# Kernel optimization log

Measured on AMD Instinct MI355X. Metric: run time of the kernel, lower is better.

The kernel has to match this reference:

```python
import jax, jax.numpy as jnp
import numpy as np

NFIELD, NKER = 8, 16
B, Y, X, P, T = 32, 32, 32, 16, 8


def setup_inputs() -> dict:
    key = jax.random.key(0)
    k1, k2 = jax.random.split(key)
    fieldpatch = jax.random.normal(k1, (B, NFIELD, Y, X, P, T), dtype=jnp.float32)
    quadpatch = jax.random.uniform(k2, (B, Y, X, P, T), dtype=jnp.float32)
    zeros_fk = jnp.zeros((NFIELD, NKER), dtype=jnp.float32)
    return {
        "fieldpatch": fieldpatch,
        "quadpatch": quadpatch,
        "mean_lat": zeros_fk, "logstd_lat": zeros_fk,
        "mean_lon": zeros_fk, "logstd_lon": zeros_fk,
        "mean_lev": zeros_fk, "logstd_lev": zeros_fk,
        "logtau_time": zeros_fk,
    }


def _gaussian1d(mean, logstd, length):
    # (f, k, length): exp(-0.5*((coord - mean)/std)^2), coord in [-1, 1]
    coord = jnp.linspace(-1.0, 1.0, length, dtype=mean.dtype)
    std = jnp.exp(logstd)
    z = (coord[None, None, :] - mean[..., None]) / std[..., None]
    return jnp.exp(-0.5 * z * z)


def _exponential1d(logtau, length):
    # (f, k, length): exp(-coord / tau), coord = 0..length-1
    coord = jnp.arange(length, dtype=logtau.dtype)
    tau = jnp.exp(logtau) + 1e-4
    return jnp.exp(-coord[None, None, :] / tau[..., None])


def reference(fieldpatch, quadpatch, mean_lat, logstd_lat, mean_lon, logstd_lon,
              mean_lev, logstd_lev, logtau_time):
    b, f, y, x, p, t = fieldpatch.shape
    ky = _gaussian1d(mean_lat, logstd_lat, y)      # (f,k,y)
    kx = _gaussian1d(mean_lon, logstd_lon, x)      # (f,k,x)
    kp = _gaussian1d(mean_lev, logstd_lev, p)      # (f,k,p)
    kt = _exponential1d(logtau_time, t)            # (f,k,t)
    # Separable outer product -> full kernel (f,k,y,x,p,t)
    kernel = jnp.einsum('fky,fkx,fkp,fkt->fkyxpt', ky, kx, kp, kt)
    qmean = quadpatch.mean(axis=0)                 # (y,x,p,t)
    integral = jnp.einsum('fkyxpt,yxpt->fk', kernel, qmean) + 1e-4
    weights = kernel / integral[:, :, None, None, None, None]
    # torch weights() runs under @torch.no_grad(): weights are constant wrt autograd
    weights = jax.lax.stop_gradient(weights)
    features = jnp.einsum('bfyxpt,fkyxpt,byxpt->bfk', fieldpatch, weights, quadpatch)
    return features.reshape(b, -1)
```

## Files before the change

### kernel.cpp

```cpp
#include <hip/hip_runtime.h>
#include <math.h>

#define NF 8
#define NK 16
#define BB 32
#define YY 32
#define XX 32
#define PP 16
#define TT 8
#define YX (YY*XX)
#define PT (PP*TT)
#define YXPT (YX*PT)
#define CHUNKS 8
#define COLS_PER_BLOCK (YX/CHUNKS)
#define COLS_PER_WAVE  (COLS_PER_BLOCK/4)
#define MAIN_ITERS     (COLS_PER_WAVE/2)

#define WPT_OFF   0
#define WYX_OFF   (NF*NK*PT)
#define QMEAN_OFF (WYX_OFF + NF*YX*NK)
#define ACC_OFF   (QMEAN_OFF + YXPT)
#define INTG_OFF  (ACC_OFF + CHUNKS*BB*NF*NK)

__global__ __launch_bounds__(256) void k_prep(const float* __restrict__ quad,
                       const float* __restrict__ mean_lat, const float* __restrict__ logstd_lat,
                       const float* __restrict__ mean_lon, const float* __restrict__ logstd_lon,
                       const float* __restrict__ mean_lev, const float* __restrict__ logstd_lev,
                       const float* __restrict__ logtau,
                       float* __restrict__ ws) {
    const int tid = threadIdx.x, bx = blockIdx.x;

    if (bx < 512) {
        __shared__ float4 sm[256];
        const int j4 = bx * 64 + (tid & 63);
        const int bg = tid >> 6;
        const float4* q4 = (const float4*)quad;
        float4 a = make_float4(0.f, 0.f, 0.f, 0.f);
        #pragma unroll
        for (int i = 0; i < 8; ++i) {
            float4 v = q4[(size_t)(bg * 8 + i) * (YXPT / 4) + j4];
            a.x += v.x; a.y += v.y; a.z += v.z; a.w += v.w;
        }
        sm[tid] = a;
        __syncthreads();
        if (tid < 64) {
            float4 r0 = sm[tid], r1 = sm[tid + 64], r2 = sm[tid + 128], r3 = sm[tid + 192];
            float4 r;
            r.x = (r0.x + r1.x + r2.x + r3.x) * (1.f / BB);
            r.y = (r0.y + r1.y + r2.y + r3.y) * (1.f / BB);
            r.z = (r0.z + r1.z + r2.z + r3.z) * (1.f / BB);
            r.w = (r0.w + r1.w + r2.w + r3.w) * (1.f / BB);
            ((float4*)(ws + QMEAN_OFF))[j4] = r;
        }
        return;
    }
    const int fk = bx - 512;
    if (tid >= 128) return;
    const int f = fk >> 4, k = fk & 15;
    const float mlat = mean_lat[fk], slat = expf(logstd_lat[fk]);
    const float mlon = mean_lon[fk], slon = expf(logstd_lon[fk]);
    const float mlev = mean_lev[fk], slev = expf(logstd_lev[fk]);
    const float tau  = expf(logtau[fk]) + 1e-4f;

    {
        const int p = tid >> 3, t = tid & 7;
        const float cp = -1.f + 2.f * (float)p / (PP - 1);
        const float zp = (cp - mlev) / slev;
        ws[WPT_OFF + fk * PT + tid] = expf(-0.5f * zp * zp) * expf(-(float)t / tau);
    }
    #pragma unroll
    for (int i = 0; i < 8; ++i) {
        const int yx = i * 128 + tid;
        const int y = yx >> 5, x = yx & 31;
        const float cy = -1.f + 2.f * (float)y / (YY - 1);
        const float cx = -1.f + 2.f * (float)x / (XX - 1);
        const float zy = (cy - mlat) / slat;
        const float zx = (cx - mlon) / slon;
        ws[WYX_OFF + (f * YX + yx) * NK + k] = expf(-0.5f * zy * zy) * expf(-0.5f * zx * zx);
    }
}

__global__ __launch_bounds__(256) void k_integral(float* __restrict__ ws) {
    const int fk = blockIdx.x >> 2, qr = blockIdx.x & 3;
    const int tid = threadIdx.x;
    const int f = fk >> 4, k = fk & 15;
    const int yx = qr * 256 + tid;
    const float4* w4 = (const float4*)(ws + WPT_OFF + fk * PT);
    const float4* q4 = (const float4*)(ws + QMEAN_OFF + (size_t)yx * PT);
    float s = 0.f;
    #pragma unroll
    for (int j = 0; j < PT / 4; ++j) {
        float4 w = w4[j], q = q4[j];
        s += w.x * q.x + w.y * q.y + w.z * q.z + w.w * q.w;
    }
    float partial = ws[WYX_OFF + (f * YX + yx) * NK + k] * s;
    #pragma unroll
    for (int m = 32; m; m >>= 1) partial += __shfl_xor(partial, m);
    __shared__ float red[4];
    if ((tid & 63) == 0) red[tid >> 6] = partial;
    __syncthreads();
    if (tid == 0)
        ws[INTG_OFF + qr * (NF * NK) + fk] = red[0] + red[1] + red[2] + red[3];
}

__global__ __launch_bounds__(256, 3) void k_main(const float* __restrict__ field,
                                                 const float* __restrict__ quad,
                                                 float* __restrict__ ws) {
    const int bx = blockIdx.x;
    const int f = bx & 7, chunk = (bx >> 3) & 7, b = bx >> 6;
    const int tid = threadIdx.x;
    const int wave = tid >> 6, L = tid & 63;
    const int half = L >> 5, qg = L & 31;

    __shared__ float sw[COLS_PER_BLOCK * NK];
    {
        const float4* src = (const float4*)(ws + WYX_OFF + (size_t)(f * YX + chunk * COLS_PER_BLOCK) * NK);
        float4* dst = (float4*)sw;
        dst[tid] = src[tid];
        dst[tid + 256] = src[tid + 256];
    }

    float4 wf[NK];
    #pragma unroll
    for (int k = 0; k < NK; ++k)
        wf[k] = *(const float4*)(ws + WPT_OFF + (f * NK + k) * PT + 4 * qg);

    float acc[NK];
    #pragma unroll
    for (int k = 0; k < NK; ++k) acc[k] = 0.f;

    const int colBase = chunk * COLS_PER_BLOCK + wave * COLS_PER_WAVE;
    const float4* fp = (const float4*)(field + (size_t)(b * NF + f) * YXPT + (size_t)colBase * PT + 4 * L);
    const float4* qp = (const float4*)(quad + (size_t)b * YXPT + (size_t)colBase * PT + 4 * L);
    const int STEP = (2 * PT) / 4;

    __syncthreads();
    const float* swc = sw + (wave * COLS_PER_WAVE + half) * NK;

    float4 fa = fp[0];
    float4 qa = qp[0];
    float4 fb = fp[STEP];
    float4 qb = qp[STEP];
    float4 fc = fp[2 * STEP];
    float4 qc = qp[2 * STEP];

    #pragma unroll 1
    for (int s = 0; s < MAIN_ITERS; ++s) {
        const int sn = (s + 3 < MAIN_ITERS) ? (s + 3) : 0;
        float4 fd = fp[sn * STEP];
        float4 qd = qp[sn * STEP];

        float4 ga;
        ga.x = fa.x * qa.x; ga.y = fa.y * qa.y; ga.z = fa.z * qa.z; ga.w = fa.w * qa.w;

        const float4* wvp = (const float4*)(swc + s * 2 * NK);
        #pragma unroll
        for (int j = 0; j < 4; ++j) {
            float4 w = wvp[j];
            {
                const int k = 4 * j;
                float d = ga.x * wf[k].x;
                d = fmaf(ga.y, wf[k].y, d);
                d = fmaf(ga.z, wf[k].z, d);
                d = fmaf(ga.w, wf[k].w, d);
                acc[k] = fmaf(w.x, d, acc[k]);
            }
            {
                const int k = 4 * j + 1;
                float d = ga.x * wf[k].x;
                d = fmaf(ga.y, wf[k].y, d);
                d = fmaf(ga.z, wf[k].z, d);
                d = fmaf(ga.w, wf[k].w, d);
                acc[k] = fmaf(w.y, d, acc[k]);
            }
            {
                const int k = 4 * j + 2;
                float d = ga.x * wf[k].x;
                d = fmaf(ga.y, wf[k].y, d);
                d = fmaf(ga.z, wf[k].z, d);
                d = fmaf(ga.w, wf[k].w, d);
                acc[k] = fmaf(w.z, d, acc[k]);
            }
            {
                const int k = 4 * j + 3;
                float d = ga.x * wf[k].x;
                d = fmaf(ga.y, wf[k].y, d);
                d = fmaf(ga.z, wf[k].z, d);
                d = fmaf(ga.w, wf[k].w, d);
                acc[k] = fmaf(w.w, d, acc[k]);
            }
        }
        fa = fb; qa = qb;
        fb = fc; qb = qc;
        fc = fd; qc = qd;
    }

    __shared__ float red[4][NK];
    #pragma unroll
    for (int k = 0; k < NK; ++k) {
        float v = acc[k];
        v += __shfl_xor(v, 32); v += __shfl_xor(v, 16); v += __shfl_xor(v, 8);
        v += __shfl_xor(v, 4);  v += __shfl_xor(v, 2);  v += __shfl_xor(v, 1);
        if (L == 0) red[wave][k] = v;
    }
    __syncthreads();
    if (tid < NK) {
        float s2 = red[0][tid] + red[1][tid] + red[2][tid] + red[3][tid];
        ws[ACC_OFF + chunk * (BB * NF * NK) + (b * NF + f) * NK + tid] = s2;
    }
}

__global__ void k_final(const float* __restrict__ ws, float* __restrict__ out) {
    int i = blockIdx.x * 256 + threadIdx.x;
    if (i >= BB * NF * NK) return;
    float a = 0.f;
    #pragma unroll
    for (int c = 0; c < CHUNKS; ++c) a += ws[ACC_OFF + c * (BB * NF * NK) + i];
    const int fk = i & (NF * NK - 1);
    float g = 1e-4f;
    #pragma unroll
    for (int q = 0; q < 4; ++q) g += ws[INTG_OFF + q * (NF * NK) + fk];
    out[i] = a / g;
}

extern "C" void kernel_launch(void* const* d_in, const int* in_sizes, int n_in,
                              void* d_out, int out_size, void* d_ws, size_t ws_size,
                              hipStream_t stream) {
    const float* field = (const float*)d_in[0];
    const float* quad  = (const float*)d_in[1];
    float* ws = (float*)d_ws;

    k_prep<<<640, 256, 0, stream>>>(quad,
        (const float*)d_in[2], (const float*)d_in[3],
        (const float*)d_in[4], (const float*)d_in[5],
        (const float*)d_in[6], (const float*)d_in[7],
        (const float*)d_in[8], ws);
    k_integral<<<NF * NK * 4, 256, 0, stream>>>(ws);
    k_main<<<BB * NF * CHUNKS, 256, 0, stream>>>(field, quad, ws);
    k_final<<<(BB * NF * NK + 255) / 256, 256, 0, stream>>>(ws, (float*)d_out);
}
```

Before: 238.6 us.

## Fuse kernel generation and normalization integral into main reduction kernel

```diff
diff --git a/kernel.cpp b/kernel.cpp
--- a/kernel.cpp
+++ b/kernel.cpp
@@ -15,212 +15,157 @@
 #define COLS_PER_BLOCK (YX/CHUNKS)
 #define COLS_PER_WAVE  (COLS_PER_BLOCK/4)
 #define MAIN_ITERS     (COLS_PER_WAVE/2)
+#define STEP           ((2*PT)/4)
 
-#define WPT_OFF   0
-#define WYX_OFF   (NF*NK*PT)
-#define QMEAN_OFF (WYX_OFF + NF*YX*NK)
-#define ACC_OFF   (QMEAN_OFF + YXPT)
-#define INTG_OFF  (ACC_OFF + CHUNKS*BB*NF*NK)
+#define ACC_OFF   0
+#define ACCQ_OFF  (CHUNKS*BB*NF*NK)
 
-__global__ __launch_bounds__(256) void k_prep(const float* __restrict__ quad,
-                       const float* __restrict__ mean_lat, const float* __restrict__ logstd_lat,
-                       const float* __restrict__ mean_lon, const float* __restrict__ logstd_lon,
-                       const float* __restrict__ mean_lev, const float* __restrict__ logstd_lev,
-                       const float* __restrict__ logtau,
-                       float* __restrict__ ws) {
-    const int tid = threadIdx.x, bx = blockIdx.x;
 
-    if (bx < 512) {
-        __shared__ float4 sm[256];
-        const int j4 = bx * 64 + (tid & 63);
-        const int bg = tid >> 6;
-        const float4* q4 = (const float4*)quad;
-        float4 a = make_float4(0.f, 0.f, 0.f, 0.f);
-        #pragma unroll
-        for (int i = 0; i < 8; ++i) {
-            float4 v = q4[(size_t)(bg * 8 + i) * (YXPT / 4) + j4];
-            a.x += v.x; a.y += v.y; a.z += v.z; a.w += v.w;
-        }
-        sm[tid] = a;
-        __syncthreads();
-        if (tid < 64) {
-            float4 r0 = sm[tid], r1 = sm[tid + 64], r2 = sm[tid + 128], r3 = sm[tid + 192];
-            float4 r;
-            r.x = (r0.x + r1.x + r2.x + r3.x) * (1.f / BB);
-            r.y = (r0.y + r1.y + r2.y + r3.y) * (1.f / BB);
-            r.z = (r0.z + r1.z + r2.z + r3.z) * (1.f / BB);
-            r.w = (r0.w + r1.w + r2.w + r3.w) * (1.f / BB);
-            ((float4*)(ws + QMEAN_OFF))[j4] = r;
-        }
-        return;
-    }
-    const int fk = bx - 512;
-    if (tid >= 128) return;
-    const int f = fk >> 4, k = fk & 15;
-    const float mlat = mean_lat[fk], slat = expf(logstd_lat[fk]);
-    const float mlon = mean_lon[fk], slon = expf(logstd_lon[fk]);
-    const float mlev = mean_lev[fk], slev = expf(logstd_lev[fk]);
-    const float tau  = expf(logtau[fk]) + 1e-4f;
+#define KQ(WC, K) do {                                                          \
+    float d  = ga.x * wf[K].x; d  = fmaf(ga.y, wf[K].y, d );                    \
+    d  = fmaf(ga.z, wf[K].z, d ); d  = fmaf(ga.w, wf[K].w, d );                 \
+    float dq = qa.x * wf[K].x; dq = fmaf(qa.y, wf[K].y, dq);                    \
+    dq = fmaf(qa.z, wf[K].z, dq); dq = fmaf(qa.w, wf[K].w, dq);                 \
+    acc[K]  = fmaf(WC, d,  acc[K]);                                             \
+    accq[K] = fmaf(WC, dq, accq[K]);                                            \
+} while (0)
 
-    {
-        const int p = tid >> 3, t = tid & 7;
-        const float cp = -1.f + 2.f * (float)p / (PP - 1);
-        const float zp = (cp - mlev) / slev;
-        ws[WPT_OFF + fk * PT + tid] = expf(-0.5f * zp * zp) * expf(-(float)t / tau);
-    }
-    #pragma unroll
-    for (int i = 0; i < 8; ++i) {
-        const int yx = i * 128 + tid;
-        const int y = yx >> 5, x = yx & 31;
-        const float cy = -1.f + 2.f * (float)y / (YY - 1);
-        const float cx = -1.f + 2.f * (float)x / (XX - 1);
-        const float zy = (cy - mlat) / slat;
-        const float zx = (cx - mlon) / slon;
-        ws[WYX_OFF + (f * YX + yx) * NK + k] = expf(-0.5f * zy * zy) * expf(-0.5f * zx * zx);
-    }
-}
+#define COLPAIR_COMPUTE(WVP) do {                                               \
+    float4 ga;                                                                  \
+    ga.x = fa.x*qa.x; ga.y = fa.y*qa.y; ga.z = fa.z*qa.z; ga.w = fa.w*qa.w;     \
+    float4 w0 = (WVP)[0], w1 = (WVP)[1], w2 = (WVP)[2], w3 = (WVP)[3];          \
+    KQ(w0.x, 0);  KQ(w0.y, 1);  KQ(w0.z, 2);  KQ(w0.w, 3);                      \
+    KQ(w1.x, 4);  KQ(w1.y, 5);  KQ(w1.z, 6);  KQ(w1.w, 7);                      \
+    KQ(w2.x, 8);  KQ(w2.y, 9);  KQ(w2.z, 10); KQ(w2.w, 11);                     \
+    KQ(w3.x, 12); KQ(w3.y, 13); KQ(w3.z, 14); KQ(w3.w, 15);                     \
+} while (0)
 
-__global__ __launch_bounds__(256) void k_integral(float* __restrict__ ws) {
-    const int fk = blockIdx.x >> 2, qr = blockIdx.x & 3;
-    const int tid = threadIdx.x;
-    const int f = fk >> 4, k = fk & 15;
-    const int yx = qr * 256 + tid;
-    const float4* w4 = (const float4*)(ws + WPT_OFF + fk * PT);
-    const float4* q4 = (const float4*)(ws + QMEAN_OFF + (size_t)yx * PT);
-    float s = 0.f;
-    #pragma unroll
-    for (int j = 0; j < PT / 4; ++j) {
-        float4 w = w4[j], q = q4[j];
-        s += w.x * q.x + w.y * q.y + w.z * q.z + w.w * q.w;
-    }
-    float partial = ws[WYX_OFF + (f * YX + yx) * NK + k] * s;
-    #pragma unroll
-    for (int m = 32; m; m >>= 1) partial += __shfl_xor(partial, m);
-    __shared__ float red[4];
-    if ((tid & 63) == 0) red[tid >> 6] = partial;
-    __syncthreads();
-    if (tid == 0)
-        ws[INTG_OFF + qr * (NF * NK) + fk] = red[0] + red[1] + red[2] + red[3];
-}
-
-__global__ __launch_bounds__(256, 3) void k_main(const float* __restrict__ field,
-                                                 const float* __restrict__ quad,
-                                                 float* __restrict__ ws) {
+__global__ __launch_bounds__(256, 3) void k_main(
+    const float* __restrict__ field, const float* __restrict__ quad,
+    const float* __restrict__ mean_lat, const float* __restrict__ logstd_lat,
+    const float* __restrict__ mean_lon, const float* __restrict__ logstd_lon,
+    const float* __restrict__ mean_lev, const float* __restrict__ logstd_lev,
+    const float* __restrict__ logtau, float* __restrict__ ws)
+{
     const int bx = blockIdx.x;
     const int f = bx & 7, chunk = (bx >> 3) & 7, b = bx >> 6;
     const int tid = threadIdx.x;
     const int wave = tid >> 6, L = tid & 63;
     const int half = L >> 5, qg = L & 31;
 
-    __shared__ float sw[COLS_PER_BLOCK * NK];
-    {
-        const float4* src = (const float4*)(ws + WYX_OFF + (size_t)(f * YX + chunk * COLS_PER_BLOCK) * NK);
-        float4* dst = (float4*)sw;
-        dst[tid] = src[tid];
-        dst[tid + 256] = src[tid + 256];
+    const int colBase = chunk * COLS_PER_BLOCK + wave * COLS_PER_WAVE;
+    const float4* fp = (const float4*)(field + (size_t)(b * NF + f) * YXPT + (size_t)colBase * PT) + L;
+    const float4* qp = (const float4*)(quad  + (size_t)b * YXPT            + (size_t)colBase * PT) + L;
+
+    float4 fbuf[4], qbuf[4];
+    #pragma unroll
+    for (int j = 0; j < 4; ++j) { fbuf[j] = fp[j * STEP]; qbuf[j] = qp[j * STEP]; }
+
+    __shared__ __align__(16) float sw[COLS_PER_BLOCK * NK];
+    __shared__ __align__(16) float spt[NK * PT];
+    __shared__ float prm[NK][8];
+
+    if (tid < NK) {
+        const int fk = f * NK + tid;
+        prm[tid][0] = mean_lat[fk];
+        prm[tid][1] = expf(-logstd_lat[fk]);
+        prm[tid][2] = mean_lon[fk];
+        prm[tid][3] = expf(-logstd_lon[fk]);
+        prm[tid][4] = mean_lev[fk];
+        prm[tid][5] = expf(-logstd_lev[fk]);
+        prm[tid][6] = 1.f / (expf(logtau[fk]) + 1e-4f);
     }
+    __syncthreads();
+
+    #pragma unroll
+    for (int i = 0; i < 8; ++i) {
+        const int e = i * 256 + tid;
+        const int col = e >> 4, k = e & 15;
+        const int yx = chunk * COLS_PER_BLOCK + col;
+        const float cy = -1.f + 2.f * (float)(yx >> 5) / (YY - 1);
+        const float cx = -1.f + 2.f * (float)(yx & 31) / (XX - 1);
+        const float zy = (cy - prm[k][0]) * prm[k][1];
+        const float zx = (cx - prm[k][2]) * prm[k][3];
+        sw[col * NK + k] = expf(-0.5f * (zy * zy + zx * zx));
+    }
+    #pragma unroll
+    for (int i = 0; i < 8; ++i) {
+        const int e = i * 256 + tid;
+        const int k = e >> 7, pt = e & 127;
+        const float cp = -1.f + 2.f * (float)(pt >> 3) / (PP - 1);
+        const float zp = (cp - prm[k][4]) * prm[k][5];
+        spt[e] = expf(-0.5f * zp * zp - (float)(pt & 7) * prm[k][6]);
+    }
+    __syncthreads();
 
     float4 wf[NK];
     #pragma unroll
-    for (int k = 0; k < NK; ++k)
-        wf[k] = *(const float4*)(ws + WPT_OFF + (f * NK + k) * PT + 4 * qg);
+    for (int k = 0; k < NK; ++k) wf[k] = ((const float4*)(spt + k * PT))[qg];
 
-    float acc[NK];
+    float acc[NK], accq[NK];
     #pragma unroll
-    for (int k = 0; k < NK; ++k) acc[k] = 0.f;
+    for (int k = 0; k < NK; ++k) { acc[k] = 0.f; accq[k] = 0.f; }
 
-    const int colBase = chunk * COLS_PER_BLOCK + wave * COLS_PER_WAVE;
-    const float4* fp = (const float4*)(field + (size_t)(b * NF + f) * YXPT + (size_t)colBase * PT + 4 * L);
-    const float4* qp = (const float4*)(quad + (size_t)b * YXPT + (size_t)colBase * PT + 4 * L);
-    const int STEP = (2 * PT) / 4;
-
-    __syncthreads();
-    const float* swc = sw + (wave * COLS_PER_WAVE + half) * NK;
-
-    float4 fa = fp[0];
-    float4 qa = qp[0];
-    float4 fb = fp[STEP];
-    float4 qb = qp[STEP];
-    float4 fc = fp[2 * STEP];
-    float4 qc = qp[2 * STEP];
+    const float* swp = sw + (wave * COLS_PER_WAVE + half) * NK;
 
     #pragma unroll 1
-    for (int s = 0; s < MAIN_ITERS; ++s) {
-        const int sn = (s + 3 < MAIN_ITERS) ? (s + 3) : 0;
-        float4 fd = fp[sn * STEP];
-        float4 qd = qp[sn * STEP];
-
-        float4 ga;
-        ga.x = fa.x * qa.x; ga.y = fa.y * qa.y; ga.z = fa.z * qa.z; ga.w = fa.w * qa.w;
-
-        const float4* wvp = (const float4*)(swc + s * 2 * NK);
+    for (int so = 0; so < 3; ++so) {
+        fp += 4 * STEP; qp += 4 * STEP;
         #pragma unroll
         for (int j = 0; j < 4; ++j) {
-            float4 w = wvp[j];
-            {
-                const int k = 4 * j;
-                float d = ga.x * wf[k].x;
-                d = fmaf(ga.y, wf[k].y, d);
-                d = fmaf(ga.z, wf[k].z, d);
-                d = fmaf(ga.w, wf[k].w, d);
-                acc[k] = fmaf(w.x, d, acc[k]);
-            }
-            {
-                const int k = 4 * j + 1;
-                float d = ga.x * wf[k].x;
-                d = fmaf(ga.y, wf[k].y, d);
-                d = fmaf(ga.z, wf[k].z, d);
-                d = fmaf(ga.w, wf[k].w, d);
-                acc[k] = fmaf(w.y, d, acc[k]);
-            }
-            {
-                const int k = 4 * j + 2;
-                float d = ga.x * wf[k].x;
-                d = fmaf(ga.y, wf[k].y, d);
-                d = fmaf(ga.z, wf[k].z, d);
-                d = fmaf(ga.w, wf[k].w, d);
-                acc[k] = fmaf(w.z, d, acc[k]);
-            }
-            {
-                const int k = 4 * j + 3;
-                float d = ga.x * wf[k].x;
-                d = fmaf(ga.y, wf[k].y, d);
-                d = fmaf(ga.z, wf[k].z, d);
-                d = fmaf(ga.w, wf[k].w, d);
-                acc[k] = fmaf(w.w, d, acc[k]);
-            }
+            float4 fa = fbuf[j], qa = qbuf[j];
+            fbuf[j] = fp[j * STEP]; qbuf[j] = qp[j * STEP];
+            const float4* wvp = (const float4*)(swp + j * (2 * NK));
+            COLPAIR_COMPUTE(wvp);
         }
-        fa = fb; qa = qb;
-        fb = fc; qb = qc;
-        fc = fd; qc = qd;
+        swp += 4 * (2 * NK);
+    }
+    #pragma unroll
+    for (int j = 0; j < 4; ++j) {
+        float4 fa = fbuf[j], qa = qbuf[j];
+        const float4* wvp = (const float4*)(swp + j * (2 * NK));
+        COLPAIR_COMPUTE(wvp);
     }
 
-    __shared__ float red[4][NK];
+    __shared__ float red[4][NK], redq[4][NK];
     #pragma unroll
     for (int k = 0; k < NK; ++k) {
         float v = acc[k];
         v += __shfl_xor(v, 32); v += __shfl_xor(v, 16); v += __shfl_xor(v, 8);
         v += __shfl_xor(v, 4);  v += __shfl_xor(v, 2);  v += __shfl_xor(v, 1);
-        if (L == 0) red[wave][k] = v;
+        float vq = accq[k];
+        vq += __shfl_xor(vq, 32); vq += __shfl_xor(vq, 16); vq += __shfl_xor(vq, 8);
+        vq += __shfl_xor(vq, 4);  vq += __shfl_xor(vq, 2);  vq += __shfl_xor(vq, 1);
+        if (L == 0) { red[wave][k] = v; redq[wave][k] = vq; }
     }
     __syncthreads();
     if (tid < NK) {
         float s2 = red[0][tid] + red[1][tid] + red[2][tid] + red[3][tid];
         ws[ACC_OFF + chunk * (BB * NF * NK) + (b * NF + f) * NK + tid] = s2;
+    } else if (tid >= 64 && tid < 64 + NK) {
+        const int k = tid - 64;
+        float s2 = redq[0][k] + redq[1][k] + redq[2][k] + redq[3][k];
+        ws[ACCQ_OFF + (chunk * BB + b) * (NF * NK) + f * NK + k] = s2;
     }
 }
 
-__global__ void k_final(const float* __restrict__ ws, float* __restrict__ out) {
-    int i = blockIdx.x * 256 + threadIdx.x;
-    if (i >= BB * NF * NK) return;
+__global__ __launch_bounds__(256) void k_final(const float* __restrict__ ws,
+                                               float* __restrict__ out) {
+    __shared__ float intg[NF * NK];
+    const int tid = threadIdx.x;
+    const int i = blockIdx.x * 256 + tid;
+    if (tid < NF * NK) {
+        float g = 0.f;
+        #pragma unroll 8
+        for (int cb = 0; cb < CHUNKS * BB; ++cb)
+            g += ws[ACCQ_OFF + cb * (NF * NK) + tid];
+        intg[tid] = 1e-4f + g * (1.f / BB);
+    }
+    __syncthreads();
     float a = 0.f;
     #pragma unroll
     for (int c = 0; c < CHUNKS; ++c) a += ws[ACC_OFF + c * (BB * NF * NK) + i];
-    const int fk = i & (NF * NK - 1);
-    float g = 1e-4f;
-    #pragma unroll
-    for (int q = 0; q < 4; ++q) g += ws[INTG_OFF + q * (NF * NK) + fk];
-    out[i] = a / g;
+    out[i] = a / intg[i & (NF * NK - 1)];
 }
 
 extern "C" void kernel_launch(void* const* d_in, const int* in_sizes, int n_in,
@@ -230,12 +175,10 @@
     const float* quad  = (const float*)d_in[1];
     float* ws = (float*)d_ws;
 
-    k_prep<<<640, 256, 0, stream>>>(quad,
+    k_main<<<BB * NF * CHUNKS, 256, 0, stream>>>(field, quad,
         (const float*)d_in[2], (const float*)d_in[3],
         (const float*)d_in[4], (const float*)d_in[5],
         (const float*)d_in[6], (const float*)d_in[7],
         (const float*)d_in[8], ws);
-    k_integral<<<NF * NK * 4, 256, 0, stream>>>(ws);
-    k_main<<<BB * NF * CHUNKS, 256, 0, stream>>>(field, quad, ws);
-    k_final<<<(BB * NF * NK + 255) / 256, 256, 0, stream>>>(ws, (float*)d_out);
+    k_final<<<(BB * NF * NK) / 256, 256, 0, stream>>>(ws, (float*)d_out);
 }
```

Result: slower. 462.5 us (+93.8%).
